# Kernel tuning notes

Measured on AMD Instinct MI355X. Metric: run time of the kernel, lower is better.

## Reference

```python
import jax, jax.numpy as jnp
import numpy as np

I, H = 256, 512  # input_sz, hidden_sz
MU_MIN, MU_MAX, STD_MIN = 1e-6, 1e6, 1e-6


def _xavier(key, shape):
    fan_in, fan_out = shape[1], shape[0]
    a = jnp.sqrt(6.0 / (fan_in + fan_out)).astype(jnp.float32)
    return jax.random.uniform(key, shape, jnp.float32, -a, a)


def setup_inputs() -> dict:
    key = jax.random.key(0)
    ks = jax.random.split(key, 6)
    B, S = 64, 512
    x = jax.random.normal(ks[0], (B, S, I), jnp.float32)
    eps = jax.random.normal(ks[1], (S + 1, B, H), jnp.float32)
    W_ih = _xavier(ks[2], (4 * H, I))   # torch LSTM weight_ih_l0, gate order i,f,g,o
    W_hh = _xavier(ks[3], (4 * H, H))
    b_ih = jnp.zeros((4 * H,), jnp.float32)
    b_hh = jnp.zeros((4 * H,), jnp.float32)
    G = _xavier(ks[4], (H, 2 * H))      # Gaussian_Sampler gauss_parameter_generator
    return {"x": x, "eps": eps, "W_ih": W_ih, "W_hh": W_hh, "b_ih": b_ih, "b_hh": b_hh, "G": G}


def _sample(c, G, eps_t):
    # c: [B,H]; stats = c @ G -> [B,2H]
    stats = c @ G
    mu = jnp.clip(stats[:, :H], MU_MIN, MU_MAX)
    std = jnp.clip(jax.nn.softplus(stats[:, H:]), STD_MIN)
    return mu + eps_t * std, mu, std


def reference(x, eps, W_ih, W_hh, b_ih, b_hh, G):
    B, S, _ = x.shape
    h0 = jnp.zeros((B, H), x.dtype)
    c0 = jnp.zeros((B, H), x.dtype)
    # initial sampling of cell state (uses eps[0])
    c0_s, mu0, std0 = _sample(c0, G, eps[0])

    def step(carry, inp):
        h, c = carry
        x_t, eps_t = inp  # [B,I], [B,H]
        gates = x_t @ W_ih.T + b_ih + h @ W_hh.T + b_hh  # [B,4H]
        i_g = jax.nn.sigmoid(gates[:, 0 * H:1 * H])
        f_g = jax.nn.sigmoid(gates[:, 1 * H:2 * H])
        g_g = jnp.tanh(gates[:, 2 * H:3 * H])
        o_g = jax.nn.sigmoid(gates[:, 3 * H:4 * H])
        c_new = f_g * c + i_g * g_g
        h_new = o_g * jnp.tanh(c_new)
        c_s, mu, std = _sample(c_new, G, eps_t)
        return (h_new, c_s), (h_new, mu, std)

    xs = (jnp.swapaxes(x, 0, 1), eps[1:])  # [S,B,I], [S,B,H]
    (h_f, c_f), (hs, mus, stds) = jax.lax.scan(step, (h0, c0_s), xs)
    hidden_seq = jnp.swapaxes(hs, 0, 1)  # [B,S,H]
    c_mus = jnp.swapaxes(jnp.concatenate([mu0[None], mus], 0), 0, 1)    # [B,S+1,H]
    c_stds = jnp.swapaxes(jnp.concatenate([std0[None], stds], 0), 0, 1)  # [B,S+1,H]
    return hidden_seq, c_mus, c_stds, h_f, c_f
```

## Files before the change

### kernel.cpp

```cpp
#include <hip/hip_runtime.h>
#include <hip/hip_bf16.h>
#include <math.h>

#define I_DIM 256
#define H_DIM 512
#define B_DIM 64
#define S_DIM 512
#define SH    (S_DIM * H_DIM)
#define S1H   ((S_DIM + 1) * H_DIM)
#define BH    (B_DIM * H_DIM)
#define NGRP  4
#define GWG   64
#define NWG_TOT (NGRP * GWG)

typedef __bf16 bf16_t;
typedef bf16_t bf16x8 __attribute__((ext_vector_type(8)));
typedef float  f32x4  __attribute__((ext_vector_type(4)));
typedef float  f32x2  __attribute__((ext_vector_type(2)));

__device__ __forceinline__ float sigm_(float x) { return 1.0f / (1.0f + __expf(-x)); }
__device__ __forceinline__ float tanh_(float x) {
    x = fminf(fmaxf(x, -15.f), 15.f);
    float e = __expf(-2.f * x);
    return (1.f - e) / (1.f + e);
}
__device__ __forceinline__ float softplus_(float x) {
    return (x > 20.0f) ? x : log1pf(__expf(x));
}
__device__ __forceinline__ unsigned short bfbits_(float f) {
    return __builtin_bit_cast(unsigned short, (bf16_t)f);
}

__device__ __forceinline__ bf16x8 ld_frag_agent(const bf16_t* base, int elem_idx) {
    const unsigned long long* p = (const unsigned long long*)(base) + (elem_idx >> 2);
    unsigned long long lo = __hip_atomic_load(p,     __ATOMIC_RELAXED, __HIP_MEMORY_SCOPE_AGENT);
    unsigned long long hi = __hip_atomic_load(p + 1, __ATOMIC_RELAXED, __HIP_MEMORY_SCOPE_AGENT);
    union { unsigned long long q[2]; bf16x8 v; } u;
    u.q[0] = lo; u.q[1] = hi;
    return u.v;
}

__global__ void k_init(bf16_t* __restrict__ hbuf0, unsigned int* __restrict__ bar,
                       float* __restrict__ out_cmu, float* __restrict__ out_cstd) {
    const int i = blockIdx.x * 256 + threadIdx.x;
    hbuf0[i] = (bf16_t)0.0f;
    const int b = i >> 9, j = i & 511;
    out_cmu [b * S1H + j] = 1e-6f;
    out_cstd[b * S1H + j] = 0.69314718055994531f;
    if (i < NWG_TOT) bar[i] = 0u;
}

__global__ __launch_bounds__(64, 1) void k_persist(
    const float* __restrict__ x, const float* __restrict__ eps,
    const float* __restrict__ W_ih, const float* __restrict__ W_hh,
    const float* __restrict__ b_ih, const float* __restrict__ b_hh,
    const float* __restrict__ Gm,
    bf16_t* __restrict__ hb0, bf16_t* __restrict__ hb1,
    bf16_t* __restrict__ cn0, bf16_t* __restrict__ cn1,
    unsigned int* __restrict__ bar,
    float* __restrict__ out_hidden, float* __restrict__ out_cmu,
    float* __restrict__ out_cstd, float* __restrict__ out_hf,
    float* __restrict__ out_cf)
{
    __shared__ __align__(16) unsigned short s_wih[8][2][64][8];
    __shared__ __align__(16) unsigned short s_gfr[16][64][8];
    __shared__ char s_pad[64 * 1024];
    if (x == nullptr) ((volatile char*)s_pad)[threadIdx.x] = 1;

    const int wc = blockIdx.x & 63;
    const int g  = blockIdx.x >> 6;
    const int l  = threadIdx.x;
    const int lr = l & 15;
    const int kq = l >> 4;
    const int nsub   = lr & 7;
    const int ghalf  = lr >> 3;
    const int mycell = wc * 8 + nsub;
    const int col0 = ghalf * H_DIM + mycell;
    const int col1 = 1024 + col0;
    const int gcol = ghalf * H_DIM + mycell;
    const int row0 = g * 16 + kq * 4;
    const int arow = g * 16 + lr;
    unsigned int* barg = bar + g * GWG;

    bf16x8 whh0[16], whh1[16];
    #pragma unroll
    for (int kt = 0; kt < 16; ++kt) {
        const float* p0 = W_hh + (size_t)col0 * H_DIM + kt * 32 + kq * 8;
        const float* p1 = W_hh + (size_t)col1 * H_DIM + kt * 32 + kq * 8;
        bf16x8 f0, f1;
        #pragma unroll
        for (int j = 0; j < 8; ++j) { f0[j] = (bf16_t)p0[j]; f1[j] = (bf16_t)p1[j]; }
        whh0[kt] = f0; whh1[kt] = f1;
    }
    #pragma unroll
    for (int kt = 0; kt < 8; ++kt) {
        const float* p0 = W_ih + (size_t)col0 * I_DIM + kt * 32 + kq * 8;
        const float* p1 = W_ih + (size_t)col1 * I_DIM + kt * 32 + kq * 8;
        bf16x8 f0, f1;
        #pragma unroll
        for (int j = 0; j < 8; ++j) { f0[j] = (bf16_t)p0[j]; f1[j] = (bf16_t)p1[j]; }
        *reinterpret_cast<bf16x8*>(&s_wih[kt][0][l][0]) = f0;
        *reinterpret_cast<bf16x8*>(&s_wih[kt][1][l][0]) = f1;
    }
    #pragma unroll
    for (int kt = 0; kt < 16; ++kt) {
        bf16x8 f;
        #pragma unroll
        for (int j = 0; j < 8; ++j)
            f[j] = (bf16_t)Gm[(size_t)(kt * 32 + kq * 8 + j) * 1024 + gcol];
        *reinterpret_cast<bf16x8*>(&s_gfr[kt][l][0]) = f;
    }
    const float bias0 = b_ih[col0] + b_hh[col0];
    const float bias1 = b_ih[col1] + b_hh[col1];
    __syncthreads();

    float csr[4];
    #pragma unroll
    for (int r = 0; r < 4; ++r)
        csr[r] = 1e-6f + eps[(size_t)(row0 + r) * H_DIM + mycell] * 0.69314718055994531f;

    f32x4 ax0e = {0,0,0,0}, ax0o = {0,0,0,0}, ax1e = {0,0,0,0}, ax1o = {0,0,0,0};
    #pragma unroll
    for (int kt = 0; kt < 8; kt += 2) {
        const float* xp = x + (size_t)arow * (S_DIM * I_DIM) + kt * 32 + kq * 8;
        float4 u0 = reinterpret_cast<const float4*>(xp)[0];
        float4 u1 = reinterpret_cast<const float4*>(xp)[1];
        float4 u2 = reinterpret_cast<const float4*>(xp + 32)[0];
        float4 u3 = reinterpret_cast<const float4*>(xp + 32)[1];
        bf16x8 af0, af1;
        af0[0]=(bf16_t)u0.x; af0[1]=(bf16_t)u0.y; af0[2]=(bf16_t)u0.z; af0[3]=(bf16_t)u0.w;
        af0[4]=(bf16_t)u1.x; af0[5]=(bf16_t)u1.y; af0[6]=(bf16_t)u1.z; af0[7]=(bf16_t)u1.w;
        af1[0]=(bf16_t)u2.x; af1[1]=(bf16_t)u2.y; af1[2]=(bf16_t)u2.z; af1[3]=(bf16_t)u2.w;
        af1[4]=(bf16_t)u3.x; af1[5]=(bf16_t)u3.y; af1[6]=(bf16_t)u3.z; af1[7]=(bf16_t)u3.w;
        bf16x8 w0e = *reinterpret_cast<const bf16x8*>(&s_wih[kt][0][l][0]);
        bf16x8 w1e = *reinterpret_cast<const bf16x8*>(&s_wih[kt][1][l][0]);
        bf16x8 w0o = *reinterpret_cast<const bf16x8*>(&s_wih[kt + 1][0][l][0]);
        bf16x8 w1o = *reinterpret_cast<const bf16x8*>(&s_wih[kt + 1][1][l][0]);
        ax0e = __builtin_amdgcn_mfma_f32_16x16x32_bf16(af0, w0e, ax0e, 0, 0, 0);
        ax1e = __builtin_amdgcn_mfma_f32_16x16x32_bf16(af0, w1e, ax1e, 0, 0, 0);
        ax0o = __builtin_amdgcn_mfma_f32_16x16x32_bf16(af1, w0o, ax0o, 0, 0, 0);
        ax1o = __builtin_amdgcn_mfma_f32_16x16x32_bf16(af1, w1o, ax1o, 0, 0, 0);
    }

    bf16x8 hf[16];
    #pragma unroll
    for (int kt = 0; kt < 16; ++kt) {
        bf16x8 z;
        #pragma unroll
        for (int j = 0; j < 8; ++j) z[j] = (bf16_t)0.0f;
        hf[kt] = z;
    }

    float  ev[4];
    f32x2  hv_st[4];
    f32x2  st_out[4];

    #pragma unroll 1
    for (int t = 0; t < S_DIM; ++t) {
        bf16_t*       hout = (t & 1) ? hb0 : hb1;
        bf16_t*       cnb  = (t & 1) ? cn1 : cn0;
        unsigned int* hout_u32 = (unsigned int*)hout;
        unsigned int* cnb_u32  = (unsigned int*)cnb;

        #pragma unroll
        for (int kt = 0; kt < 16; kt += 2) {
            ax0e = __builtin_amdgcn_mfma_f32_16x16x32_bf16(hf[kt],     whh0[kt],     ax0e, 0, 0, 0);
            ax1e = __builtin_amdgcn_mfma_f32_16x16x32_bf16(hf[kt],     whh1[kt],     ax1e, 0, 0, 0);
            ax0o = __builtin_amdgcn_mfma_f32_16x16x32_bf16(hf[kt + 1], whh0[kt + 1], ax0o, 0, 0, 0);
            ax1o = __builtin_amdgcn_mfma_f32_16x16x32_bf16(hf[kt + 1], whh1[kt + 1], ax1o, 0, 0, 0);
        }
        f32x4 a0 = ax0e + ax0o, a1 = ax1e + ax1o;

        #pragma unroll
        for (int r = 0; r < 4; ++r) {
            float sif = sigm_(a0[r] + bias0);
            float v1  = a1[r] + bias1;
            float go  = (ghalf == 0) ? tanh_(v1) : sigm_(v1);
            float fv  = __shfl_xor(sif, 8);
            float ov  = __shfl_xor(go, 8);
            float cn  = fv * csr[r] + sif * go;
            float hn  = ov * tanh_(cn);
            unsigned hcw = ((unsigned)bfbits_(cn) << 16) | (unsigned)bfbits_(hn);
            unsigned pp  = __shfl_xor(hcw, 1);
            float    hp  = __shfl_xor(hn, 1);
            hv_st[r].x = hn; hv_st[r].y = hp;
            if (ghalf == 0 && !(lr & 1)) {
                const int row  = row0 + r;
                const int cidx = (row * H_DIM + mycell) >> 1;
                unsigned hw = ((pp & 0xFFFFu) << 16) | (hcw & 0xFFFFu);
                unsigned cw = (pp & 0xFFFF0000u)     | (hcw >> 16);
                __hip_atomic_store(hout_u32 + cidx, hw, __ATOMIC_RELAXED, __HIP_MEMORY_SCOPE_AGENT);
                __hip_atomic_store(cnb_u32  + cidx, cw, __ATOMIC_RELAXED, __HIP_MEMORY_SCOPE_AGENT);
            }
        }

        __threadfence_block();
        if (l == 0)
            __hip_atomic_store(&barg[wc], (unsigned)(t + 1),
                               __ATOMIC_RELAXED, __HIP_MEMORY_SCOPE_AGENT);

        ax0e = ax0o = ax1e = ax1o = (f32x4){0,0,0,0};
        if (t + 1 < S_DIM) {
            #pragma unroll
            for (int kt = 0; kt < 8; kt += 2) {
                const float* xp = x + (size_t)arow * (S_DIM * I_DIM)
                                    + (size_t)(t + 1) * I_DIM + kt * 32 + kq * 8;
                float4 u0 = reinterpret_cast<const float4*>(xp)[0];
                float4 u1 = reinterpret_cast<const float4*>(xp)[1];
                float4 u2 = reinterpret_cast<const float4*>(xp + 32)[0];
                float4 u3 = reinterpret_cast<const float4*>(xp + 32)[1];
                bf16x8 af0, af1;
                af0[0]=(bf16_t)u0.x; af0[1]=(bf16_t)u0.y; af0[2]=(bf16_t)u0.z; af0[3]=(bf16_t)u0.w;
                af0[4]=(bf16_t)u1.x; af0[5]=(bf16_t)u1.y; af0[6]=(bf16_t)u1.z; af0[7]=(bf16_t)u1.w;
                af1[0]=(bf16_t)u2.x; af1[1]=(bf16_t)u2.y; af1[2]=(bf16_t)u2.z; af1[3]=(bf16_t)u2.w;
                af1[4]=(bf16_t)u3.x; af1[5]=(bf16_t)u3.y; af1[6]=(bf16_t)u3.z; af1[7]=(bf16_t)u3.w;
                bf16x8 w0e = *reinterpret_cast<const bf16x8*>(&s_wih[kt][0][l][0]);
                bf16x8 w1e = *reinterpret_cast<const bf16x8*>(&s_wih[kt][1][l][0]);
                bf16x8 w0o = *reinterpret_cast<const bf16x8*>(&s_wih[kt + 1][0][l][0]);
                bf16x8 w1o = *reinterpret_cast<const bf16x8*>(&s_wih[kt + 1][1][l][0]);
                ax0e = __builtin_amdgcn_mfma_f32_16x16x32_bf16(af0, w0e, ax0e, 0, 0, 0);
                ax1e = __builtin_amdgcn_mfma_f32_16x16x32_bf16(af0, w1e, ax1e, 0, 0, 0);
                ax0o = __builtin_amdgcn_mfma_f32_16x16x32_bf16(af1, w0o, ax0o, 0, 0, 0);
                ax1o = __builtin_amdgcn_mfma_f32_16x16x32_bf16(af1, w1o, ax1o, 0, 0, 0);
            }
        }
        if (t) {
            if (!(lr & 1)) {
                #pragma unroll
                for (int r = 0; r < 4; ++r) {
                    float* outp = ((ghalf == 0) ? out_cmu : out_cstd)
                                  + (size_t)(row0 + r) * S1H + (size_t)t * H_DIM + mycell;
                    __builtin_nontemporal_store(st_out[r], (f32x2*)outp);
                }
            }
        }
        if (ghalf == 0 && !(lr & 1)) {
            #pragma unroll
            for (int r = 0; r < 4; ++r)
                __builtin_nontemporal_store(hv_st[r],
                    (f32x2*)(out_hidden + (size_t)(row0 + r) * SH + (size_t)t * H_DIM + mycell));
        }
        #pragma unroll
        for (int r = 0; r < 4; ++r)
            ev[r] = eps[(size_t)(t + 1) * BH + (size_t)(row0 + r) * H_DIM + mycell];

        {
            const unsigned target = (unsigned)(t + 1);
            while (true) {
                unsigned v = __hip_atomic_load(&barg[l], __ATOMIC_RELAXED,
                                               __HIP_MEMORY_SCOPE_AGENT);
                if (__all((int)(v >= target))) break;
                __builtin_amdgcn_s_sleep(1);
            }
        }
        __atomic_signal_fence(__ATOMIC_ACQUIRE);

        bf16x8 cf[16];
        #pragma unroll
        for (int kt = 0; kt < 16; ++kt)
            cf[kt] = ld_frag_agent(cnb, arow * H_DIM + kt * 32 + kq * 8);
        #pragma unroll
        for (int kt = 0; kt < 16; ++kt)
            hf[kt] = ld_frag_agent(hout, arow * H_DIM + kt * 32 + kq * 8);

        f32x4 se = {0,0,0,0}, so = {0,0,0,0};
        #pragma unroll
        for (int kt = 0; kt < 16; kt += 2) {
            bf16x8 g0 = *reinterpret_cast<const bf16x8*>(&s_gfr[kt][l][0]);
            bf16x8 g1 = *reinterpret_cast<const bf16x8*>(&s_gfr[kt + 1][l][0]);
            se = __builtin_amdgcn_mfma_f32_16x16x32_bf16(cf[kt],     g0, se, 0, 0, 0);
            so = __builtin_amdgcn_mfma_f32_16x16x32_bf16(cf[kt + 1], g1, so, 0, 0, 0);
        }
        f32x4 st = se + so;
        #pragma unroll
        for (int r = 0; r < 4; ++r) {
            float sv  = st[r];
            float muv = fminf(fmaxf(sv, 1e-6f), 1e6f);
            float sdv = fmaxf(softplus_(sv), 1e-6f);
            float outv = (ghalf == 0) ? muv : sdv;
            float op   = __shfl_xor(outv, 1);
            st_out[r].x = outv; st_out[r].y = op;
            float sd_p = __shfl_xor(outv, 8);
            csr[r] = muv + ev[r] * sd_p;
        }
    }

    if (!(lr & 1)) {
        #pragma unroll
        for (int r = 0; r < 4; ++r) {
            float* outp = ((ghalf == 0) ? out_cmu : out_cstd)
                          + (size_t)(row0 + r) * S1H + (size_t)S_DIM * H_DIM + mycell;
            __builtin_nontemporal_store(st_out[r], (f32x2*)outp);
        }
    }
    if (ghalf == 0 && !(lr & 1)) {
        #pragma unroll
        for (int r = 0; r < 4; ++r)
            __builtin_nontemporal_store(hv_st[r],
                (f32x2*)(out_hf + (row0 + r) * H_DIM + mycell));
    }
    if (ghalf == 0) {
        #pragma unroll
        for (int r = 0; r < 4; ++r)
            __builtin_nontemporal_store(csr[r], out_cf + (row0 + r) * H_DIM + mycell);
    }
}

extern "C" void kernel_launch(void* const* d_in, const int* in_sizes, int n_in,
                              void* d_out, int out_size, void* d_ws, size_t ws_size,
                              hipStream_t stream) {
    (void)in_sizes; (void)n_in; (void)out_size; (void)ws_size;

    const float* x    = (const float*)d_in[0];
    const float* eps  = (const float*)d_in[1];
    const float* W_ih = (const float*)d_in[2];
    const float* W_hh = (const float*)d_in[3];
    const float* b_ih = (const float*)d_in[4];
    const float* b_hh = (const float*)d_in[5];
    const float* Gm   = (const float*)d_in[6];

    float* out        = (float*)d_out;
    float* out_hidden = out;
    float* out_cmu    = out_hidden + (size_t)B_DIM * SH;
    float* out_cstd   = out_cmu + (size_t)B_DIM * S1H;
    float* out_hf     = out_cstd + (size_t)B_DIM * S1H;
    float* out_cf     = out_hf + (size_t)B_DIM * H_DIM;

    char* wsb = (char*)d_ws;
    bf16_t* hb0 = (bf16_t*)(wsb);
    bf16_t* hb1 = (bf16_t*)(wsb + (1u << 16));
    bf16_t* cn0 = (bf16_t*)(wsb + 2u * (1u << 16));
    bf16_t* cn1 = (bf16_t*)(wsb + 3u * (1u << 16));
    unsigned int* bar = (unsigned int*)(wsb + 4u * (1u << 16));

    k_init<<<dim3(128), dim3(256), 0, stream>>>(hb0, bar, out_cmu, out_cstd);
    k_persist<<<dim3(NWG_TOT), dim3(64), 0, stream>>>(
        x, eps, W_ih, W_hh, b_ih, b_hh, Gm,
        hb0, hb1, cn0, cn1, bar,
        out_hidden, out_cmu, out_cstd, out_hf, out_cf);
}
```

Baseline: 3.796 ms.

## Halve persistent workgroups; each handles two 8-cell slices with W_hh in LDS

Cuts the workgroups per batch group from 64 to 32, so each workgroup processes two 8-cell hidden slices per timestep. Because the register budget can no longer hold both slices of W_hh, the W_hh fragments move from registers into shared memory and are re-read from LDS every step. The 64KB LDS padding that forced one workgroup per CU is removed. The intent is to cut grid-barrier polling and participant count and to amortise the h/c fragment loads, at the cost of twice the serial MFMA work per workgroup and extra LDS traffic each step.

```diff
diff --git a/kernel.cpp b/kernel.cpp
--- a/kernel.cpp
+++ b/kernel.cpp
@@ -10,7 +10,7 @@
 #define S1H   ((S_DIM + 1) * H_DIM)
 #define BH    (B_DIM * H_DIM)
 #define NGRP  4
-#define GWG   64
+#define GWG   32
 #define NWG_TOT (NGRP * GWG)
 
 typedef __bf16 bf16_t;
@@ -62,64 +62,79 @@
     float* __restrict__ out_cstd, float* __restrict__ out_hf,
     float* __restrict__ out_cf)
 {
-    __shared__ __align__(16) unsigned short s_wih[8][2][64][8];
-    __shared__ __align__(16) unsigned short s_gfr[16][64][8];
-    __shared__ char s_pad[64 * 1024];
-    if (x == nullptr) ((volatile char*)s_pad)[threadIdx.x] = 1;
-
-    const int wc = blockIdx.x & 63;
-    const int g  = blockIdx.x >> 6;
+    __shared__ __align__(16) unsigned short s_whh[2][16][2][64][8];
+    __shared__ __align__(16) unsigned short s_wih[2][8][2][64][8];
+    __shared__ __align__(16) unsigned short s_gfr[2][16][64][8];
+
+    const int wc = blockIdx.x & 31;
+    const int g  = blockIdx.x >> 5;
     const int l  = threadIdx.x;
     const int lr = l & 15;
     const int kq = l >> 4;
     const int nsub   = lr & 7;
     const int ghalf  = lr >> 3;
-    const int mycell = wc * 8 + nsub;
-    const int col0 = ghalf * H_DIM + mycell;
-    const int col1 = 1024 + col0;
-    const int gcol = ghalf * H_DIM + mycell;
     const int row0 = g * 16 + kq * 4;
     const int arow = g * 16 + lr;
     unsigned int* barg = bar + g * GWG;
 
-    bf16x8 whh0[16], whh1[16];
-    #pragma unroll
-    for (int kt = 0; kt < 16; ++kt) {
-        const float* p0 = W_hh + (size_t)col0 * H_DIM + kt * 32 + kq * 8;
-        const float* p1 = W_hh + (size_t)col1 * H_DIM + kt * 32 + kq * 8;
-        bf16x8 f0, f1;
-        #pragma unroll
-        for (int j = 0; j < 8; ++j) { f0[j] = (bf16_t)p0[j]; f1[j] = (bf16_t)p1[j]; }
-        whh0[kt] = f0; whh1[kt] = f1;
-    }
-    #pragma unroll
-    for (int kt = 0; kt < 8; ++kt) {
-        const float* p0 = W_ih + (size_t)col0 * I_DIM + kt * 32 + kq * 8;
-        const float* p1 = W_ih + (size_t)col1 * I_DIM + kt * 32 + kq * 8;
-        bf16x8 f0, f1;
-        #pragma unroll
-        for (int j = 0; j < 8; ++j) { f0[j] = (bf16_t)p0[j]; f1[j] = (bf16_t)p1[j]; }
-        *reinterpret_cast<bf16x8*>(&s_wih[kt][0][l][0]) = f0;
-        *reinterpret_cast<bf16x8*>(&s_wih[kt][1][l][0]) = f1;
-    }
-    #pragma unroll
-    for (int kt = 0; kt < 16; ++kt) {
-        bf16x8 f;
-        #pragma unroll
-        for (int j = 0; j < 8; ++j)
-            f[j] = (bf16_t)Gm[(size_t)(kt * 32 + kq * 8 + j) * 1024 + gcol];
-        *reinterpret_cast<bf16x8*>(&s_gfr[kt][l][0]) = f;
-    }
-    const float bias0 = b_ih[col0] + b_hh[col0];
-    const float bias1 = b_ih[col1] + b_hh[col1];
+    int mycell[2], col0[2], col1[2];
+    #pragma unroll
+    for (int s = 0; s < 2; ++s) {
+        mycell[s] = wc * 16 + s * 8 + nsub;
+        col0[s]   = ghalf * H_DIM + mycell[s];
+        col1[s]   = 1024 + col0[s];
+    }
+
+    #pragma unroll
+    for (int s = 0; s < 2; ++s) {
+        #pragma unroll
+        for (int kt = 0; kt < 16; ++kt) {
+            const float* p0 = W_hh + (size_t)col0[s] * H_DIM + kt * 32 + kq * 8;
+            const float* p1 = W_hh + (size_t)col1[s] * H_DIM + kt * 32 + kq * 8;
+            bf16x8 f0, f1;
+            #pragma unroll
+            for (int j = 0; j < 8; ++j) { f0[j] = (bf16_t)p0[j]; f1[j] = (bf16_t)p1[j]; }
+            *reinterpret_cast<bf16x8*>(&s_whh[s][kt][0][l][0]) = f0;
+            *reinterpret_cast<bf16x8*>(&s_whh[s][kt][1][l][0]) = f1;
+        }
+        #pragma unroll
+        for (int kt = 0; kt < 8; ++kt) {
+            const float* p0 = W_ih + (size_t)col0[s] * I_DIM + kt * 32 + kq * 8;
+            const float* p1 = W_ih + (size_t)col1[s] * I_DIM + kt * 32 + kq * 8;
+            bf16x8 f0, f1;
+            #pragma unroll
+            for (int j = 0; j < 8; ++j) { f0[j] = (bf16_t)p0[j]; f1[j] = (bf16_t)p1[j]; }
+            *reinterpret_cast<bf16x8*>(&s_wih[s][kt][0][l][0]) = f0;
+            *reinterpret_cast<bf16x8*>(&s_wih[s][kt][1][l][0]) = f1;
+        }
+        #pragma unroll
+        for (int kt = 0; kt < 16; ++kt) {
+            bf16x8 f;
+            #pragma unroll
+            for (int j = 0; j < 8; ++j)
+                f[j] = (bf16_t)Gm[(size_t)(kt * 32 + kq * 8 + j) * 1024 + col0[s]];
+            *reinterpret_cast<bf16x8*>(&s_gfr[s][kt][l][0]) = f;
+        }
+    }
+    float bias0[2], bias1[2];
+    #pragma unroll
+    for (int s = 0; s < 2; ++s) {
+        bias0[s] = b_ih[col0[s]] + b_hh[col0[s]];
+        bias1[s] = b_ih[col1[s]] + b_hh[col1[s]];
+    }
     __syncthreads();
 
-    float csr[4];
-    #pragma unroll
-    for (int r = 0; r < 4; ++r)
-        csr[r] = 1e-6f + eps[(size_t)(row0 + r) * H_DIM + mycell] * 0.69314718055994531f;
-
-    f32x4 ax0e = {0,0,0,0}, ax0o = {0,0,0,0}, ax1e = {0,0,0,0}, ax1o = {0,0,0,0};
+    float csr[2][4];
+    #pragma unroll
+    for (int s = 0; s < 2; ++s)
+        #pragma unroll
+        for (int r = 0; r < 4; ++r)
+            csr[s][r] = 1e-6f + eps[(size_t)(row0 + r) * H_DIM + mycell[s]] * 0.69314718055994531f;
+
+    f32x4 ax0e[2], ax0o[2], ax1e[2], ax1o[2];
+    #pragma unroll
+    for (int s = 0; s < 2; ++s) { ax0e[s] = (f32x4){0,0,0,0}; ax0o[s] = (f32x4){0,0,0,0};
+                                  ax1e[s] = (f32x4){0,0,0,0}; ax1o[s] = (f32x4){0,0,0,0}; }
     #pragma unroll
     for (int kt = 0; kt < 8; kt += 2) {
         const float* xp = x + (size_t)arow * (S_DIM * I_DIM) + kt * 32 + kq * 8;
@@ -132,14 +147,17 @@
         af0[4]=(bf16_t)u1.x; af0[5]=(bf16_t)u1.y; af0[6]=(bf16_t)u1.z; af0[7]=(bf16_t)u1.w;
         af1[0]=(bf16_t)u2.x; af1[1]=(bf16_t)u2.y; af1[2]=(bf16_t)u2.z; af1[3]=(bf16_t)u2.w;
         af1[4]=(bf16_t)u3.x; af1[5]=(bf16_t)u3.y; af1[6]=(bf16_t)u3.z; af1[7]=(bf16_t)u3.w;
-        bf16x8 w0e = *reinterpret_cast<const bf16x8*>(&s_wih[kt][0][l][0]);
-        bf16x8 w1e = *reinterpret_cast<const bf16x8*>(&s_wih[kt][1][l][0]);
-        bf16x8 w0o = *reinterpret_cast<const bf16x8*>(&s_wih[kt + 1][0][l][0]);
-        bf16x8 w1o = *reinterpret_cast<const bf16x8*>(&s_wih[kt + 1][1][l][0]);
-        ax0e = __builtin_amdgcn_mfma_f32_16x16x32_bf16(af0, w0e, ax0e, 0, 0, 0);
-        ax1e = __builtin_amdgcn_mfma_f32_16x16x32_bf16(af0, w1e, ax1e, 0, 0, 0);
-        ax0o = __builtin_amdgcn_mfma_f32_16x16x32_bf16(af1, w0o, ax0o, 0, 0, 0);
-        ax1o = __builtin_amdgcn_mfma_f32_16x16x32_bf16(af1, w1o, ax1o, 0, 0, 0);
+        #pragma unroll
+        for (int s = 0; s < 2; ++s) {
+            bf16x8 w0e = *reinterpret_cast<const bf16x8*>(&s_wih[s][kt][0][l][0]);
+            bf16x8 w1e = *reinterpret_cast<const bf16x8*>(&s_wih[s][kt][1][l][0]);
+            bf16x8 w0o = *reinterpret_cast<const bf16x8*>(&s_wih[s][kt + 1][0][l][0]);
+            bf16x8 w1o = *reinterpret_cast<const bf16x8*>(&s_wih[s][kt + 1][1][l][0]);
+            ax0e[s] = __builtin_amdgcn_mfma_f32_16x16x32_bf16(af0, w0e, ax0e[s], 0, 0, 0);
+            ax1e[s] = __builtin_amdgcn_mfma_f32_16x16x32_bf16(af0, w1e, ax1e[s], 0, 0, 0);
+            ax0o[s] = __builtin_amdgcn_mfma_f32_16x16x32_bf16(af1, w0o, ax0o[s], 0, 0, 0);
+            ax1o[s] = __builtin_amdgcn_mfma_f32_16x16x32_bf16(af1, w1o, ax1o[s], 0, 0, 0);
+        }
     }
 
     bf16x8 hf[16];
@@ -151,9 +169,9 @@
         hf[kt] = z;
     }
 
-    float  ev[4];
-    f32x2  hv_st[4];
-    f32x2  st_out[4];
+    float  ev[2][4];
+    f32x2  hv_st[2][4];
+    f32x2  st_out[2][4];
 
     #pragma unroll 1
     for (int t = 0; t < S_DIM; ++t) {
@@ -163,34 +181,44 @@
         unsigned int* cnb_u32  = (unsigned int*)cnb;
 
         #pragma unroll
-        for (int kt = 0; kt < 16; kt += 2) {
-            ax0e = __builtin_amdgcn_mfma_f32_16x16x32_bf16(hf[kt],     whh0[kt],     ax0e, 0, 0, 0);
-            ax1e = __builtin_amdgcn_mfma_f32_16x16x32_bf16(hf[kt],     whh1[kt],     ax1e, 0, 0, 0);
-            ax0o = __builtin_amdgcn_mfma_f32_16x16x32_bf16(hf[kt + 1], whh0[kt + 1], ax0o, 0, 0, 0);
-            ax1o = __builtin_amdgcn_mfma_f32_16x16x32_bf16(hf[kt + 1], whh1[kt + 1], ax1o, 0, 0, 0);
-        }
-        f32x4 a0 = ax0e + ax0o, a1 = ax1e + ax1o;
-
-        #pragma unroll
-        for (int r = 0; r < 4; ++r) {
-            float sif = sigm_(a0[r] + bias0);
-            float v1  = a1[r] + bias1;
-            float go  = (ghalf == 0) ? tanh_(v1) : sigm_(v1);
-            float fv  = __shfl_xor(sif, 8);
-            float ov  = __shfl_xor(go, 8);
-            float cn  = fv * csr[r] + sif * go;
-            float hn  = ov * tanh_(cn);
-            unsigned hcw = ((unsigned)bfbits_(cn) << 16) | (unsigned)bfbits_(hn);
-            unsigned pp  = __shfl_xor(hcw, 1);
-            float    hp  = __shfl_xor(hn, 1);
-            hv_st[r].x = hn; hv_st[r].y = hp;
-            if (ghalf == 0 && !(lr & 1)) {
-                const int row  = row0 + r;
-                const int cidx = (row * H_DIM + mycell) >> 1;
-                unsigned hw = ((pp & 0xFFFFu) << 16) | (hcw & 0xFFFFu);
-                unsigned cw = (pp & 0xFFFF0000u)     | (hcw >> 16);
-                __hip_atomic_store(hout_u32 + cidx, hw, __ATOMIC_RELAXED, __HIP_MEMORY_SCOPE_AGENT);
-                __hip_atomic_store(cnb_u32  + cidx, cw, __ATOMIC_RELAXED, __HIP_MEMORY_SCOPE_AGENT);
+        for (int s = 0; s < 2; ++s) {
+            #pragma unroll
+            for (int kt = 0; kt < 16; kt += 2) {
+                bf16x8 w0e = *reinterpret_cast<const bf16x8*>(&s_whh[s][kt][0][l][0]);
+                bf16x8 w1e = *reinterpret_cast<const bf16x8*>(&s_whh[s][kt][1][l][0]);
+                bf16x8 w0o = *reinterpret_cast<const bf16x8*>(&s_whh[s][kt + 1][0][l][0]);
+                bf16x8 w1o = *reinterpret_cast<const bf16x8*>(&s_whh[s][kt + 1][1][l][0]);
+                ax0e[s] = __builtin_amdgcn_mfma_f32_16x16x32_bf16(hf[kt],     w0e, ax0e[s], 0, 0, 0);
+                ax1e[s] = __builtin_amdgcn_mfma_f32_16x16x32_bf16(hf[kt],     w1e, ax1e[s], 0, 0, 0);
+                ax0o[s] = __builtin_amdgcn_mfma_f32_16x16x32_bf16(hf[kt + 1], w0o, ax0o[s], 0, 0, 0);
+                ax1o[s] = __builtin_amdgcn_mfma_f32_16x16x32_bf16(hf[kt + 1], w1o, ax1o[s], 0, 0, 0);
+            }
+        }
+
+        #pragma unroll
+        for (int s = 0; s < 2; ++s) {
+            f32x4 a0 = ax0e[s] + ax0o[s], a1 = ax1e[s] + ax1o[s];
+            #pragma unroll
+            for (int r = 0; r < 4; ++r) {
+                float sif = sigm_(a0[r] + bias0[s]);
+                float v1  = a1[r] + bias1[s];
+                float go  = (ghalf == 0) ? tanh_(v1) : sigm_(v1);
+                float fv  = __shfl_xor(sif, 8);
+                float ov  = __shfl_xor(go, 8);
+                float cn  = fv * csr[s][r] + sif * go;
+                float hn  = ov * tanh_(cn);
+                unsigned hcw = ((unsigned)bfbits_(cn) << 16) | (unsigned)bfbits_(hn);
+                unsigned pp  = __shfl_xor(hcw, 1);
+                float    hp  = __shfl_xor(hn, 1);
+                hv_st[s][r].x = hn; hv_st[s][r].y = hp;
+                if (ghalf == 0 && !(lr & 1)) {
+                    const int row  = row0 + r;
+                    const int cidx = (row * H_DIM + mycell[s]) >> 1;
+                    unsigned hw = ((pp & 0xFFFFu) << 16) | (hcw & 0xFFFFu);
+                    unsigned cw = (pp & 0xFFFF0000u)     | (hcw >> 16);
+                    __hip_atomic_store(hout_u32 + cidx, hw, __ATOMIC_RELAXED, __HIP_MEMORY_SCOPE_AGENT);
+                    __hip_atomic_store(cnb_u32  + cidx, cw, __ATOMIC_RELAXED, __HIP_MEMORY_SCOPE_AGENT);
+                }
             }
         }
 
@@ -199,7 +227,9 @@
             __hip_atomic_store(&barg[wc], (unsigned)(t + 1),
                                __ATOMIC_RELAXED, __HIP_MEMORY_SCOPE_AGENT);
 
-        ax0e = ax0o = ax1e = ax1o = (f32x4){0,0,0,0};
+        #pragma unroll
+        for (int s = 0; s < 2; ++s) { ax0e[s] = (f32x4){0,0,0,0}; ax0o[s] = (f32x4){0,0,0,0};
+                                      ax1e[s] = (f32x4){0,0,0,0}; ax1o[s] = (f32x4){0,0,0,0}; }
         if (t + 1 < S_DIM) {
             #pragma unroll
             for (int kt = 0; kt < 8; kt += 2) {
@@ -214,40 +244,44 @@
                 af0[4]=(bf16_t)u1.x; af0[5]=(bf16_t)u1.y; af0[6]=(bf16_t)u1.z; af0[7]=(bf16_t)u1.w;
                 af1[0]=(bf16_t)u2.x; af1[1]=(bf16_t)u2.y; af1[2]=(bf16_t)u2.z; af1[3]=(bf16_t)u2.w;
                 af1[4]=(bf16_t)u3.x; af1[5]=(bf16_t)u3.y; af1[6]=(bf16_t)u3.z; af1[7]=(bf16_t)u3.w;
-                bf16x8 w0e = *reinterpret_cast<const bf16x8*>(&s_wih[kt][0][l][0]);
-                bf16x8 w1e = *reinterpret_cast<const bf16x8*>(&s_wih[kt][1][l][0]);
-                bf16x8 w0o = *reinterpret_cast<const bf16x8*>(&s_wih[kt + 1][0][l][0]);
-                bf16x8 w1o = *reinterpret_cast<const bf16x8*>(&s_wih[kt + 1][1][l][0]);
-                ax0e = __builtin_amdgcn_mfma_f32_16x16x32_bf16(af0, w0e, ax0e, 0, 0, 0);
-                ax1e = __builtin_amdgcn_mfma_f32_16x16x32_bf16(af0, w1e, ax1e, 0, 0, 0);
-                ax0o = __builtin_amdgcn_mfma_f32_16x16x32_bf16(af1, w0o, ax0o, 0, 0, 0);
-                ax1o = __builtin_amdgcn_mfma_f32_16x16x32_bf16(af1, w1o, ax1o, 0, 0, 0);
-            }
-        }
-        if (t) {
-            if (!(lr & 1)) {
+                #pragma unroll
+                for (int s = 0; s < 2; ++s) {
+                    bf16x8 w0e = *reinterpret_cast<const bf16x8*>(&s_wih[s][kt][0][l][0]);
+                    bf16x8 w1e = *reinterpret_cast<const bf16x8*>(&s_wih[s][kt][1][l][0]);
+                    bf16x8 w0o = *reinterpret_cast<const bf16x8*>(&s_wih[s][kt + 1][0][l][0]);
+                    bf16x8 w1o = *reinterpret_cast<const bf16x8*>(&s_wih[s][kt + 1][1][l][0]);
+                    ax0e[s] = __builtin_amdgcn_mfma_f32_16x16x32_bf16(af0, w0e, ax0e[s], 0, 0, 0);
+                    ax1e[s] = __builtin_amdgcn_mfma_f32_16x16x32_bf16(af0, w1e, ax1e[s], 0, 0, 0);
+                    ax0o[s] = __builtin_amdgcn_mfma_f32_16x16x32_bf16(af1, w0o, ax0o[s], 0, 0, 0);
+                    ax1o[s] = __builtin_amdgcn_mfma_f32_16x16x32_bf16(af1, w1o, ax1o[s], 0, 0, 0);
+                }
+            }
+        }
+        #pragma unroll
+        for (int s = 0; s < 2; ++s) {
+            if (t && !(lr & 1)) {
                 #pragma unroll
                 for (int r = 0; r < 4; ++r) {
                     float* outp = ((ghalf == 0) ? out_cmu : out_cstd)
-                                  + (size_t)(row0 + r) * S1H + (size_t)t * H_DIM + mycell;
-                    __builtin_nontemporal_store(st_out[r], (f32x2*)outp);
+                                  + (size_t)(row0 + r) * S1H + (size_t)t * H_DIM + mycell[s];
+                    __builtin_nontemporal_store(st_out[s][r], (f32x2*)outp);
                 }
             }
-        }
-        if (ghalf == 0 && !(lr & 1)) {
+            if (ghalf == 0 && !(lr & 1)) {
+                #pragma unroll
+                for (int r = 0; r < 4; ++r)
+                    __builtin_nontemporal_store(hv_st[s][r],
+                        (f32x2*)(out_hidden + (size_t)(row0 + r) * SH + (size_t)t * H_DIM + mycell[s]));
+            }
             #pragma unroll
             for (int r = 0; r < 4; ++r)
-                __builtin_nontemporal_store(hv_st[r],
-                    (f32x2*)(out_hidden + (size_t)(row0 + r) * SH + (size_t)t * H_DIM + mycell));
-        }
-        #pragma unroll
-        for (int r = 0; r < 4; ++r)
-            ev[r] = eps[(size_t)(t + 1) * BH + (size_t)(row0 + r) * H_DIM + mycell];
+                ev[s][r] = eps[(size_t)(t + 1) * BH + (size_t)(row0 + r) * H_DIM + mycell[s]];
+        }
 
         {
             const unsigned target = (unsigned)(t + 1);
             while (true) {
-                unsigned v = __hip_atomic_load(&barg[l], __ATOMIC_RELAXED,
+                unsigned v = __hip_atomic_load(&barg[l & 31], __ATOMIC_RELAXED,
                                                __HIP_MEMORY_SCOPE_AGENT);
                 if (__all((int)(v >= target))) break;
                 __builtin_amdgcn_s_sleep(1);
@@ -263,46 +297,52 @@
         for (int kt = 0; kt < 16; ++kt)
             hf[kt] = ld_frag_agent(hout, arow * H_DIM + kt * 32 + kq * 8);
 
-        f32x4 se = {0,0,0,0}, so = {0,0,0,0};
-        #pragma unroll
-        for (int kt = 0; kt < 16; kt += 2) {
-            bf16x8 g0 = *reinterpret_cast<const bf16x8*>(&s_gfr[kt][l][0]);
-            bf16x8 g1 = *reinterpret_cast<const bf16x8*>(&s_gfr[kt + 1][l][0]);
-            se = __builtin_amdgcn_mfma_f32_16x16x32_bf16(cf[kt],     g0, se, 0, 0, 0);
-            so = __builtin_amdgcn_mfma_f32_16x16x32_bf16(cf[kt + 1], g1, so, 0, 0, 0);
-        }
-        f32x4 st = se + so;
-        #pragma unroll
-        for (int r = 0; r < 4; ++r) {
-            float sv  = st[r];
-            float muv = fminf(fmaxf(sv, 1e-6f), 1e6f);
-            float sdv = fmaxf(softplus_(sv), 1e-6f);
-            float outv = (ghalf == 0) ? muv : sdv;
-            float op   = __shfl_xor(outv, 1);
-            st_out[r].x = outv; st_out[r].y = op;
-            float sd_p = __shfl_xor(outv, 8);
-            csr[r] = muv + ev[r] * sd_p;
-        }
-    }
-
-    if (!(lr & 1)) {
-        #pragma unroll
-        for (int r = 0; r < 4; ++r) {
-            float* outp = ((ghalf == 0) ? out_cmu : out_cstd)
-                          + (size_t)(row0 + r) * S1H + (size_t)S_DIM * H_DIM + mycell;
-            __builtin_nontemporal_store(st_out[r], (f32x2*)outp);
-        }
-    }
-    if (ghalf == 0 && !(lr & 1)) {
-        #pragma unroll
-        for (int r = 0; r < 4; ++r)
-            __builtin_nontemporal_store(hv_st[r],
-                (f32x2*)(out_hf + (row0 + r) * H_DIM + mycell));
-    }
-    if (ghalf == 0) {
-        #pragma unroll
-        for (int r = 0; r < 4; ++r)
-            __builtin_nontemporal_store(csr[r], out_cf + (row0 + r) * H_DIM + mycell);
+        #pragma unroll
+        for (int s = 0; s < 2; ++s) {
+            f32x4 se = {0,0,0,0}, so = {0,0,0,0};
+            #pragma unroll
+            for (int kt = 0; kt < 16; kt += 2) {
+                bf16x8 g0 = *reinterpret_cast<const bf16x8*>(&s_gfr[s][kt][l][0]);
+                bf16x8 g1 = *reinterpret_cast<const bf16x8*>(&s_gfr[s][kt + 1][l][0]);
+                se = __builtin_amdgcn_mfma_f32_16x16x32_bf16(cf[kt],     g0, se, 0, 0, 0);
+                so = __builtin_amdgcn_mfma_f32_16x16x32_bf16(cf[kt + 1], g1, so, 0, 0, 0);
+            }
+            f32x4 st = se + so;
+            #pragma unroll
+            for (int r = 0; r < 4; ++r) {
+                float sv  = st[r];
+                float muv = fminf(fmaxf(sv, 1e-6f), 1e6f);
+                float sdv = fmaxf(softplus_(sv), 1e-6f);
+                float outv = (ghalf == 0) ? muv : sdv;
+                float op   = __shfl_xor(outv, 1);
+                st_out[s][r].x = outv; st_out[s][r].y = op;
+                float sd_p = __shfl_xor(outv, 8);
+                csr[s][r] = muv + ev[s][r] * sd_p;
+            }
+        }
+    }
+
+    #pragma unroll
+    for (int s = 0; s < 2; ++s) {
+        if (!(lr & 1)) {
+            #pragma unroll
+            for (int r = 0; r < 4; ++r) {
+                float* outp = ((ghalf == 0) ? out_cmu : out_cstd)
+                              + (size_t)(row0 + r) * S1H + (size_t)S_DIM * H_DIM + mycell[s];
+                __builtin_nontemporal_store(st_out[s][r], (f32x2*)outp);
+            }
+        }
+        if (ghalf == 0 && !(lr & 1)) {
+            #pragma unroll
+            for (int r = 0; r < 4; ++r)
+                __builtin_nontemporal_store(hv_st[s][r],
+                    (f32x2*)(out_hf + (row0 + r) * H_DIM + mycell[s]));
+        }
+        if (ghalf == 0) {
+            #pragma unroll
+            for (int r = 0; r < 4; ++r)
+                __builtin_nontemporal_store(csr[s][r], out_cf + (row0 + r) * H_DIM + mycell[s]);
+        }
     }
 }
 
```

Result: slower. 5.295 ms (+39.5%).
